# Optimization experiments

Measured on AMD Instinct MI355X. Metric: run time of the kernel, lower is better.

Reference implementation:

```python
import jax, jax.numpy as jnp
import numpy as np

NUM_HEADS = 16
HEAD_DIM = 128
POLY_ORDER = 4
LRPE_BASE = 10000.0
EPS = 1e-6


def _rope(x, offset=0):
    # x: [b, n, h, d] -- Lrpe type-1 rotary position embedding per head dim
    d = x.shape[-1]
    half = d // 2
    theta = LRPE_BASE ** (-jnp.arange(half, dtype=jnp.float32) * 2.0 / d)  # [half]
    pos = jnp.arange(x.shape[1], dtype=jnp.float32) + offset               # [n]
    ang = pos[:, None] * theta[None, :]                                    # [n, half]
    cos = jnp.cos(ang)[None, :, None, :]
    sin = jnp.sin(ang)[None, :, None, :]
    x1, x2 = x[..., :half], x[..., half:]
    return jnp.concatenate([x1 * cos - x2 * sin, x1 * sin + x2 * cos], axis=-1)


def setup_inputs() -> dict:
    key = jax.random.key(0)
    ks = jax.random.split(key, 5)
    b, n, d = 2, 2048, 2048
    std = 0.02  # init_std from module
    x = jax.random.normal(ks[0], (b, n, d), dtype=jnp.float32)
    Wq = jax.random.normal(ks[1], (d, d), dtype=jnp.float32) * std
    Wk = jax.random.normal(ks[2], (d, d), dtype=jnp.float32) * std
    Wv = jax.random.normal(ks[3], (d, d), dtype=jnp.float32) * std
    Wo = jax.random.normal(ks[4], (d, d), dtype=jnp.float32) * std
    return {"x": x, "Wq": Wq, "Wk": Wk, "Wv": Wv, "Wo": Wo}


def reference(x, Wq, Wk, Wv, Wo):
    b, n, d = x.shape
    h, hd = NUM_HEADS, HEAD_DIM
    # projections (nn.Linear: x @ W.T)
    q = (x @ Wq.T).reshape(b, n, h, hd)
    k = (x @ Wk.T).reshape(b, n, h, hd)
    v = (x @ Wv.T).reshape(b, n, h, hd)
    # LRPE (rotary, type 1), offset = 0 (no cache)
    q = _rope(q)
    k = _rope(k)
    # polynomial (non-softmax) attention: scores = (q.k)^p, causal mask,
    # row-normalized (linear-attention-style denominator)
    scores = jnp.einsum("bnhd,bmhd->bhnm", q, k) ** POLY_ORDER  # p=4 even -> >=0
    causal = jnp.tril(jnp.ones((n, n), dtype=scores.dtype))
    scores = scores * causal
    denom = jnp.maximum(scores.sum(-1, keepdims=True), EPS)      # [b,h,n,1]
    out = jnp.einsum("bhnm,bmhd->bhnd", scores, v) / denom        # [b,h,n,hd]
    out = out.transpose(0, 2, 1, 3).reshape(b, n, d)              # b n (h d)
    return out @ Wo.T
```

## Files before the change

kernel.cpp:

```cpp
#include <hip/hip_runtime.h>


typedef __bf16 bf16;
typedef __bf16 bf16x8 __attribute__((ext_vector_type(8)));
typedef __bf16 bf16x4 __attribute__((ext_vector_type(4)));
typedef float f32x4 __attribute__((ext_vector_type(4)));

#define GLD(g, l)                                                   \
  __builtin_amdgcn_global_load_lds(                                 \
      (const __attribute__((address_space(1))) void*)(g),           \
      (__attribute__((address_space(3))) void*)(l), 16, 0, 0)

#define MFMA(a, b, c) __builtin_amdgcn_mfma_f32_16x16x32_bf16(a, b, c, 0, 0, 0)

__global__ __launch_bounds__(256) void k_prep(
    const float* __restrict__ x, const float* __restrict__ Wq,
    const float* __restrict__ Wk, const float* __restrict__ Wv,
    const float* __restrict__ Wo, bf16* __restrict__ xb,
    bf16* __restrict__ wqkv, bf16* __restrict__ wob,
    float* __restrict__ ct, float* __restrict__ st) {
  const int b = blockIdx.x, tid = threadIdx.x;
  if (b < 8192) {
    int i = b * 256 + tid;
    float4 v = reinterpret_cast<const float4*>(x)[i];
    bf16x4 o = {(bf16)v.x, (bf16)v.y, (bf16)v.z, (bf16)v.w};
    reinterpret_cast<bf16x4*>(xb)[i] = o;
  } else if (b < 20480) {
    int i = (b - 8192) * 256 + tid;
    const float* src = (i < 1048576) ? Wq : ((i < 2097152) ? Wk : Wv);
    float4 v = reinterpret_cast<const float4*>(src)[i & 1048575];
    bf16x4 o = {(bf16)v.x, (bf16)v.y, (bf16)v.z, (bf16)v.w};
    reinterpret_cast<bf16x4*>(wqkv)[i] = o;
  } else if (b < 24576) {
    int i = (b - 20480) * 256 + tid;
    float4 v = reinterpret_cast<const float4*>(Wo)[i];
    bf16x4 o = {(bf16)v.x, (bf16)v.y, (bf16)v.z, (bf16)v.w};
    reinterpret_cast<bf16x4*>(wob)[i] = o;
  } else {
    int i = (b - 24576) * 256 + tid;
    int pos = i >> 6, f = i & 63;
    float theta = exp2f(-(float)f * 0.20762050593046014f);
    float ang = (float)pos * theta;
    ct[i] = cosf(ang);
    st[i] = sinf(ang);
  }
}

__global__ __launch_bounds__(256, 2) void k_gemm_qkv(
    const bf16* __restrict__ Am, const bf16* __restrict__ Bm,
    bf16* __restrict__ Qp, bf16* __restrict__ Kp, bf16* __restrict__ Vt,
    const float* __restrict__ ct, const float* __restrict__ st) {
  __shared__ __align__(16) char LDS[73728];
  const int tid = threadIdx.x, w = tid >> 6, l = tid & 63;
  const int lr = l & 15, g = l >> 4;
  const int wr = w >> 1, wc = w & 1;
  const int tm = blockIdx.y * 256, tn = blockIdx.x * 128;

  const int rl = tid >> 2;
  const int scol = (((tid & 3) ^ (rl & 3) ^ ((rl >> 2) & 3)) << 3);
  const int xo = ((g ^ (lr & 3) ^ ((lr >> 2) & 3)) << 4);

#define STAGEQ(buf, kt)                                                      \
  {                                                                          \
    _Pragma("unroll") for (int i = 0; i < 4; ++i)                            \
        GLD(Am + (size_t)(tm + i * 64 + rl) * 2048 + (kt) + scol,            \
            LDS + (buf) * 24576 + i * 4096 + tid * 16);                      \
    _Pragma("unroll") for (int i = 0; i < 2; ++i)                            \
        GLD(Bm + (size_t)(tn + i * 64 + rl) * 2048 + (kt) + scol,            \
            LDS + (buf) * 24576 + 16384 + i * 4096 + tid * 16);              \
  }

  f32x4 acc[8][4] = {};

  STAGEQ(0, 0);
  STAGEQ(1, 32);
  int cur = 0, st3 = 2;
  for (int t = 0; t < 63; ++t) {
    asm volatile("s_waitcnt vmcnt(6)" ::: "memory");
    __builtin_amdgcn_s_barrier();
    asm volatile("" ::: "memory");
    if (t < 62) STAGEQ(st3, (t + 2) * 32);
    const char* pa = LDS + cur * 24576;
    const char* pb = pa + 16384;
    bf16x8 a[8], b[4];
#pragma unroll
    for (int fm = 0; fm < 8; ++fm)
      a[fm] = *reinterpret_cast<const bf16x8*>(pa + (wr * 128 + fm * 16 + lr) * 64 + xo);
#pragma unroll
    for (int nf = 0; nf < 4; ++nf)
      b[nf] = *reinterpret_cast<const bf16x8*>(pb + (wc * 64 + nf * 16 + lr) * 64 + xo);
    __builtin_amdgcn_s_setprio(1);
#pragma unroll
    for (int fm = 0; fm < 8; ++fm)
#pragma unroll
      for (int nf = 0; nf < 4; ++nf)
        acc[fm][nf] = MFMA(a[fm], b[nf], acc[fm][nf]);
    __builtin_amdgcn_s_setprio(0);
    cur = (cur == 2) ? 0 : cur + 1;
    st3 = (st3 == 2) ? 0 : st3 + 1;
  }
  {
    asm volatile("s_waitcnt vmcnt(0)" ::: "memory");
    __builtin_amdgcn_s_barrier();
    asm volatile("" ::: "memory");
    const char* pa = LDS + cur * 24576;
    const char* pb = pa + 16384;
    bf16x8 a[8], b[4];
#pragma unroll
    for (int fm = 0; fm < 8; ++fm)
      a[fm] = *reinterpret_cast<const bf16x8*>(pa + (wr * 128 + fm * 16 + lr) * 64 + xo);
#pragma unroll
    for (int nf = 0; nf < 4; ++nf)
      b[nf] = *reinterpret_cast<const bf16x8*>(pb + (wc * 64 + nf * 16 + lr) * 64 + xo);
#pragma unroll
    for (int fm = 0; fm < 8; ++fm)
#pragma unroll
      for (int nf = 0; nf < 4; ++nf)
        acc[fm][nf] = MFMA(a[fm], b[nf], acc[fm][nf]);
  }

  if (tn < 4096) {
    __syncthreads();
    bf16* E = (bf16*)LDS;
#pragma unroll
    for (int fm = 0; fm < 8; ++fm)
#pragma unroll
      for (int nf = 0; nf < 4; ++nf)
#pragma unroll
        for (int rr = 0; rr < 4; ++rr)
          E[(wr * 128 + fm * 16 + g * 4 + rr) * 136 + wc * 64 + nf * 16 + lr] =
              (bf16)acc[fm][nf][rr];
    __syncthreads();
    const int hh = (tn & 2047) >> 7;
    bf16* dst = (tn < 2048) ? Qp : Kp;
#pragma unroll
    for (int i = 0; i < 16; ++i) {
      int task = i * 256 + tid;
      int row = task >> 4, dg = (task & 15) << 2;
      int token = tm + row, nn = token & 2047, bb = token >> 11;
      f32x4 c4 = *reinterpret_cast<const f32x4*>(ct + nn * 64 + dg);
      f32x4 s4 = *reinterpret_cast<const f32x4*>(st + nn * 64 + dg);
      bf16x4 x1 = *reinterpret_cast<const bf16x4*>(E + row * 136 + dg);
      bf16x4 x2 = *reinterpret_cast<const bf16x4*>(E + row * 136 + 64 + dg);
      bf16x4 o1, o2;
#pragma unroll
      for (int j = 0; j < 4; ++j) {
        float a1 = (float)x1[j], a2 = (float)x2[j];
        o1[j] = (bf16)(a1 * c4[j] - a2 * s4[j]);
        o2[j] = (bf16)(a1 * s4[j] + a2 * c4[j]);
      }
      size_t rb = (((size_t)bb * 16 + hh) * 2048 + nn) * 128;
      *reinterpret_cast<bf16x4*>(dst + rb + dg) = o1;
      *reinterpret_cast<bf16x4*>(dst + rb + 64 + dg) = o2;
    }
  } else {
#pragma unroll
    for (int fm = 0; fm < 8; ++fm)
#pragma unroll
      for (int nf = 0; nf < 4; ++nf) {
        int row0 = tm + wr * 128 + fm * 16 + g * 4;
        int col = (tn - 4096) + wc * 64 + nf * 16 + lr;
        int bb = row0 >> 11, nn = row0 & 2047;
        int hh = col >> 7, dd = col & 127;
        bf16x4 o = {(bf16)acc[fm][nf][0], (bf16)acc[fm][nf][1],
                    (bf16)acc[fm][nf][2], (bf16)acc[fm][nf][3]};
        *reinterpret_cast<bf16x4*>(
            Vt + (((size_t)bb * 16 + hh) * 128 + dd) * 2048 + nn) = o;
      }
  }
}

__global__ __launch_bounds__(256, 3) void k_gemm_out(const bf16* __restrict__ Am,
                                                     const bf16* __restrict__ Bm,
                                                     float* __restrict__ C) {
  __shared__ __align__(16) char LDS[49152];
  const int tid = threadIdx.x, w = tid >> 6, l = tid & 63;
  const int lr = l & 15, g = l >> 4;
  const int wr = w >> 1, wc = w & 1;
  const int tm = blockIdx.y * 128, tn = blockIdx.x * 128;

  const int rl = tid >> 2;
  const int scol = (((tid & 3) ^ (rl & 3) ^ ((rl >> 2) & 3)) << 3);
  const int xo = ((g ^ (lr & 3) ^ ((lr >> 2) & 3)) << 4);

#define STAGEO(buf, kt)                                                      \
  {                                                                          \
    _Pragma("unroll") for (int i = 0; i < 2; ++i)                            \
        GLD(Am + (size_t)(tm + i * 64 + rl) * 2048 + (kt) + scol,            \
            LDS + (buf) * 16384 + i * 4096 + tid * 16);                      \
    _Pragma("unroll") for (int i = 0; i < 2; ++i)                            \
        GLD(Bm + (size_t)(tn + i * 64 + rl) * 2048 + (kt) + scol,            \
            LDS + (buf) * 16384 + 8192 + i * 4096 + tid * 16);               \
  }

  f32x4 acc[4][4] = {};

  STAGEO(0, 0);
  STAGEO(1, 32);
  int cur = 0, st3 = 2;
  for (int t = 0; t < 63; ++t) {
    asm volatile("s_waitcnt vmcnt(4)" ::: "memory");
    __builtin_amdgcn_s_barrier();
    asm volatile("" ::: "memory");
    if (t < 62) STAGEO(st3, (t + 2) * 32);
    const char* pa = LDS + cur * 16384;
    const char* pb = pa + 8192;
    bf16x8 a[4], b[4];
#pragma unroll
    for (int fm = 0; fm < 4; ++fm)
      a[fm] = *reinterpret_cast<const bf16x8*>(pa + (wr * 64 + fm * 16 + lr) * 64 + xo);
#pragma unroll
    for (int nf = 0; nf < 4; ++nf)
      b[nf] = *reinterpret_cast<const bf16x8*>(pb + (wc * 64 + nf * 16 + lr) * 64 + xo);
    __builtin_amdgcn_s_setprio(1);
#pragma unroll
    for (int fm = 0; fm < 4; ++fm)
#pragma unroll
      for (int nf = 0; nf < 4; ++nf)
        acc[fm][nf] = MFMA(a[fm], b[nf], acc[fm][nf]);
    __builtin_amdgcn_s_setprio(0);
    cur = (cur == 2) ? 0 : cur + 1;
    st3 = (st3 == 2) ? 0 : st3 + 1;
  }
  {
    asm volatile("s_waitcnt vmcnt(0)" ::: "memory");
    __builtin_amdgcn_s_barrier();
    asm volatile("" ::: "memory");
    const char* pa = LDS + cur * 16384;
    const char* pb = pa + 8192;
    bf16x8 a[4], b[4];
#pragma unroll
    for (int fm = 0; fm < 4; ++fm)
      a[fm] = *reinterpret_cast<const bf16x8*>(pa + (wr * 64 + fm * 16 + lr) * 64 + xo);
#pragma unroll
    for (int nf = 0; nf < 4; ++nf)
      b[nf] = *reinterpret_cast<const bf16x8*>(pb + (wc * 64 + nf * 16 + lr) * 64 + xo);
#pragma unroll
    for (int fm = 0; fm < 4; ++fm)
#pragma unroll
      for (int nf = 0; nf < 4; ++nf)
        acc[fm][nf] = MFMA(a[fm], b[nf], acc[fm][nf]);
  }

#pragma unroll
  for (int fm = 0; fm < 4; ++fm)
#pragma unroll
    for (int nf = 0; nf < 4; ++nf)
#pragma unroll
      for (int rr = 0; rr < 4; ++rr) {
        int row = tm + wr * 64 + fm * 16 + g * 4 + rr;
        int col = tn + wc * 64 + nf * 16 + lr;
        C[(size_t)row * 2048 + col] = acc[fm][nf][rr];
      }
}

__global__ __launch_bounds__(256) void k_attn(const bf16* __restrict__ Q,
                                              const bf16* __restrict__ K,
                                              const bf16* __restrict__ Vt,
                                              bf16* __restrict__ O) {
  __shared__ __align__(16) bf16 Ks[2][64 * 128];
  __shared__ __align__(16) bf16 Vs[2][128 * 64];
  __shared__ __align__(16) bf16 Ps[128 * 64];
  const int tid = threadIdx.x, w = tid >> 6, l = tid & 63;
  const int lr = l & 15, g = l >> 4;
  const int pair = blockIdx.x >> 5;
  const int bh = blockIdx.x & 31;
  const size_t base = (size_t)bh * 2048 * 128;
  const int b_ = bh >> 4, h_ = bh & 15;

  bf16x8 vones = {};
  if (lr == 0) {
#pragma unroll
    for (int j = 0; j < 8; ++j) vones[j] = (bf16)1.0f;
  }

#define STAGEKV(tt, buf)                                                 \
  {                                                                      \
    const bf16* kg = K + base + (size_t)(tt) * 64 * 128;                 \
    _Pragma("unroll") for (int r = 0; r < 4; ++r) {                      \
      int row = r * 16 + w * 4 + (l >> 4);                               \
      int cc = l & 15;                                                   \
      GLD(kg + (row << 7) + ((cc ^ (row & 7)) << 3),                     \
          Ks[buf] + r * 2048 + w * 512);                                 \
    }                                                                    \
    const bf16* vg = Vt + base + (tt) * 64;                              \
    _Pragma("unroll") for (int r = 0; r < 4; ++r) {                      \
      int row = r * 32 + w * 8 + (l >> 3);                               \
      int cc = l & 7;                                                    \
      GLD(vg + (size_t)row * 2048 + ((cc ^ (row & 7)) << 3),             \
          Vs[buf] + r * 2048 + w * 512);                                 \
    }                                                                    \
  }

  for (int seg = 0; seg < 2; ++seg) {
    const int qb = seg ? (15 - pair) : pair;
    const int qbase = qb * 128;
    const int nt = 2 * qb + 2;

    bf16x8 qf[2][4];
#pragma unroll
    for (int mi = 0; mi < 2; ++mi)
#pragma unroll
      for (int kc = 0; kc < 4; ++kc)
        qf[mi][kc] = *reinterpret_cast<const bf16x8*>(
            Q + base + (size_t)(qbase + w * 32 + mi * 16 + lr) * 128 + kc * 32 + g * 8);

    f32x4 on[2][8] = {};
    f32x4 dn4[2] = {};

    __builtin_amdgcn_s_barrier();
    STAGEKV(0, 0);

    for (int t = 0; t < nt; ++t) {
      int tn1 = (t + 1 < nt) ? t + 1 : nt - 1;
      STAGEKV(tn1, (t + 1) & 1);
      asm volatile("s_waitcnt vmcnt(8)" ::: "memory");
      __builtin_amdgcn_s_barrier();

      const bf16* kcur = Ks[t & 1];
      const bf16* vcur = Vs[t & 1];

      f32x4 s[2][4] = {};
      __builtin_amdgcn_s_setprio(1);
#pragma unroll
      for (int kc = 0; kc < 4; ++kc) {
        bf16x8 kb[4];
#pragma unroll
        for (int ni = 0; ni < 4; ++ni)
          kb[ni] = *reinterpret_cast<const bf16x8*>(
              kcur + ((ni * 16 + lr) << 7) + (((kc * 4 + g) ^ (lr & 7)) << 3));
#pragma unroll
        for (int mi = 0; mi < 2; ++mi)
#pragma unroll
          for (int ni = 0; ni < 4; ++ni)
            s[mi][ni] = MFMA(qf[mi][kc], kb[ni], s[mi][ni]);
      }
      __builtin_amdgcn_s_setprio(0);

#pragma unroll
      for (int mi = 0; mi < 2; ++mi) {
        const bool msk = (t * 64 + 63 > qbase + w * 32 + mi * 16);
#pragma unroll
        for (int ni = 0; ni < 4; ++ni)
#pragma unroll
          for (int r = 0; r < 4; ++r) {
            int lrow = mi * 16 + g * 4 + r;
            float v = s[mi][ni][r];
            if (msk) {
              int qrow = qbase + w * 32 + lrow;
              int col = t * 64 + ni * 16 + lr;
              v = (col <= qrow) ? v : 0.f;
            }
            float v2 = v * v, v4 = v2 * v2;
            Ps[((w * 32 + lrow) << 6) +
               (((ni * 2 + (lr >> 3)) ^ (lrow & 7)) << 3) + (lr & 7)] = (bf16)v4;
          }
      }

      __builtin_amdgcn_s_setprio(1);
#pragma unroll
      for (int k2 = 0; k2 < 2; ++k2) {
        bf16x8 pa[2];
#pragma unroll
        for (int mi = 0; mi < 2; ++mi)
          pa[mi] = *reinterpret_cast<const bf16x8*>(
              Ps + ((w * 32 + mi * 16 + lr) << 6) + (((k2 * 4 + g) ^ (lr & 7)) << 3));
        dn4[0] = MFMA(pa[0], vones, dn4[0]);
        dn4[1] = MFMA(pa[1], vones, dn4[1]);
#pragma unroll
        for (int ni = 0; ni < 8; ++ni) {
          bf16x8 vbf = *reinterpret_cast<const bf16x8*>(
              vcur + ((ni * 16 + lr) << 6) + (((k2 * 4 + g) ^ (lr & 7)) << 3));
          on[0][ni] = MFMA(pa[0], vbf, on[0][ni]);
          on[1][ni] = MFMA(pa[1], vbf, on[1][ni]);
        }
      }
      __builtin_amdgcn_s_setprio(0);
      __builtin_amdgcn_s_barrier();
    }

    asm volatile("s_waitcnt vmcnt(0)" ::: "memory");

#pragma unroll
    for (int mi = 0; mi < 2; ++mi)
#pragma unroll
      for (int r = 0; r < 4; ++r) {
        float d = __shfl(dn4[mi][r], l & 48);
        float inv = 1.0f / fmaxf(d, 1e-6f);
        int row = qbase + w * 32 + mi * 16 + g * 4 + r;
#pragma unroll
        for (int ni = 0; ni < 8; ++ni)
          O[((size_t)b_ * 2048 + row) * 2048 + h_ * 128 + ni * 16 + lr] =
              (bf16)(on[mi][ni][r] * inv);
      }
  }
#undef STAGEKV
}

extern "C" void kernel_launch(void* const* d_in, const int* in_sizes, int n_in,
                              void* d_out, int out_size, void* d_ws, size_t ws_size,
                              hipStream_t stream) {
  const float* x  = (const float*)d_in[0];
  const float* Wq = (const float*)d_in[1];
  const float* Wk = (const float*)d_in[2];
  const float* Wv = (const float*)d_in[3];
  const float* Wo = (const float*)d_in[4];
  float* out = (float*)d_out;

  char* p = (char*)d_ws;
  bf16* xb   = (bf16*)p; p += (size_t)8388608 * 2;
  bf16* wqkv = (bf16*)p; p += (size_t)12582912 * 2;
  bf16* wob  = (bf16*)p; p += (size_t)4194304 * 2;
  bf16* Qp   = (bf16*)p; p += (size_t)8388608 * 2;
  bf16* Kp   = (bf16*)p; p += (size_t)8388608 * 2;
  bf16* Vt   = (bf16*)p; p += (size_t)8388608 * 2;
  bf16* Ob   = (bf16*)p; p += (size_t)8388608 * 2;
  float* ct  = (float*)p; p += (size_t)131072 * 4;
  float* st  = (float*)p; p += (size_t)131072 * 4;

  k_prep<<<25088, 256, 0, stream>>>(x, Wq, Wk, Wv, Wo, xb, wqkv, wob, ct, st);

  k_gemm_qkv<<<dim3(48, 16), 256, 0, stream>>>(xb, wqkv, Qp, Kp, Vt, ct, st);

  k_attn<<<256, 256, 0, stream>>>(Qp, Kp, Vt, Ob);

  k_gemm_out<<<dim3(16, 32), 256, 0, stream>>>(Ob, wob, out);
}
```

Baseline: 243.6 us.

## Split attention KV tiles across two wave groups with LDS reduction

The attention kernel now runs 512 threads per block: two groups of four waves each process alternating 64-key tiles for the same 128 query rows, each group with its own LDS region for K, V and P. V is staged into a single buffer with an extra wait and barrier before the PV MFMAs, while K stays double-buffered. At the end, group 1 writes its partial outputs and denominators to LDS and group 0 sums them, normalizes and writes the result. This doubles the waves per block to hide latency on a 256-block grid, at the cost of 128KB of LDS per block, extra barriers and a reduction epilogue.

```diff
diff --git a/kernel.cpp b/kernel.cpp
--- a/kernel.cpp
+++ b/kernel.cpp
@@ -254,19 +254,19 @@
       }
 }
 
-__global__ __launch_bounds__(256) void k_attn(const bf16* __restrict__ Q,
+__global__ __launch_bounds__(512) void k_attn(const bf16* __restrict__ Q,
                                               const bf16* __restrict__ K,
                                               const bf16* __restrict__ Vt,
                                               bf16* __restrict__ O) {
-  __shared__ __align__(16) bf16 Ks[2][64 * 128];
-  __shared__ __align__(16) bf16 Vs[2][128 * 64];
-  __shared__ __align__(16) bf16 Ps[128 * 64];
+  __shared__ __align__(16) char LDSC[131072];
   const int tid = threadIdx.x, w = tid >> 6, l = tid & 63;
+  const int wg = w & 3, gp = w >> 2;
   const int lr = l & 15, g = l >> 4;
   const int pair = blockIdx.x >> 5;
   const int bh = blockIdx.x & 31;
   const size_t base = (size_t)bh * 2048 * 128;
   const int b_ = bh >> 4, h_ = bh & 15;
+  const int GB = gp * 65536;
 
   bf16x8 vones = {};
   if (lr == 0) {
@@ -274,28 +274,31 @@
     for (int j = 0; j < 8; ++j) vones[j] = (bf16)1.0f;
   }
 
-#define STAGEKV(tt, buf)                                                 \
-  {                                                                      \
-    const bf16* kg = K + base + (size_t)(tt) * 64 * 128;                 \
-    _Pragma("unroll") for (int r = 0; r < 4; ++r) {                      \
-      int row = r * 16 + w * 4 + (l >> 4);                               \
-      int cc = l & 15;                                                   \
-      GLD(kg + (row << 7) + ((cc ^ (row & 7)) << 3),                     \
-          Ks[buf] + r * 2048 + w * 512);                                 \
-    }                                                                    \
-    const bf16* vg = Vt + base + (tt) * 64;                              \
-    _Pragma("unroll") for (int r = 0; r < 4; ++r) {                      \
-      int row = r * 32 + w * 8 + (l >> 3);                               \
-      int cc = l & 7;                                                    \
-      GLD(vg + (size_t)row * 2048 + ((cc ^ (row & 7)) << 3),             \
-          Vs[buf] + r * 2048 + w * 512);                                 \
-    }                                                                    \
+#define STAGE_K(tt, buf)                                                  \
+  {                                                                       \
+    const bf16* kg = K + base + (size_t)(tt) * 64 * 128;                  \
+    _Pragma("unroll") for (int r = 0; r < 4; ++r) {                       \
+      int row = r * 16 + wg * 4 + (l >> 4);                               \
+      int cc = l & 15;                                                    \
+      GLD(kg + (row << 7) + ((cc ^ (row & 7)) << 3),                      \
+          LDSC + GB + (buf) * 16384 + r * 4096 + wg * 1024);              \
+    }                                                                     \
+  }
+#define STAGE_V(tt)                                                       \
+  {                                                                       \
+    const bf16* vg = Vt + base + (tt) * 64;                               \
+    _Pragma("unroll") for (int r = 0; r < 4; ++r) {                       \
+      int row = r * 32 + wg * 8 + (l >> 3);                               \
+      int cc = l & 7;                                                     \
+      GLD(vg + (size_t)row * 2048 + ((cc ^ (row & 7)) << 3),              \
+          LDSC + GB + 32768 + r * 4096 + wg * 1024);                      \
+    }                                                                     \
   }
 
   for (int seg = 0; seg < 2; ++seg) {
     const int qb = seg ? (15 - pair) : pair;
     const int qbase = qb * 128;
-    const int nt = 2 * qb + 2;
+    const int nh = qb + 1;
 
     bf16x8 qf[2][4];
 #pragma unroll
@@ -303,22 +306,25 @@
 #pragma unroll
       for (int kc = 0; kc < 4; ++kc)
         qf[mi][kc] = *reinterpret_cast<const bf16x8*>(
-            Q + base + (size_t)(qbase + w * 32 + mi * 16 + lr) * 128 + kc * 32 + g * 8);
+            Q + base + (size_t)(qbase + wg * 32 + mi * 16 + lr) * 128 + kc * 32 + g * 8);
 
     f32x4 on[2][8] = {};
     f32x4 dn4[2] = {};
 
     __builtin_amdgcn_s_barrier();
-    STAGEKV(0, 0);
-
-    for (int t = 0; t < nt; ++t) {
-      int tn1 = (t + 1 < nt) ? t + 1 : nt - 1;
-      STAGEKV(tn1, (t + 1) & 1);
+    STAGE_K(gp, 0);
+
+    for (int j = 0; j < nh; ++j) {
+      const int t = 2 * j + gp;
+      const int tnx = (j + 1 < nh) ? t + 2 : t;
+      STAGE_V(t);
+      STAGE_K(tnx, (j + 1) & 1);
       asm volatile("s_waitcnt vmcnt(8)" ::: "memory");
       __builtin_amdgcn_s_barrier();
 
-      const bf16* kcur = Ks[t & 1];
-      const bf16* vcur = Vs[t & 1];
+      const bf16* kcur = (const bf16*)(LDSC + GB + (j & 1) * 16384);
+      const bf16* vcur = (const bf16*)(LDSC + GB + 32768);
+      bf16* Ps = (bf16*)(LDSC + GB + 49152);
 
       f32x4 s[2][4] = {};
       __builtin_amdgcn_s_setprio(1);
@@ -339,7 +345,7 @@
 
 #pragma unroll
       for (int mi = 0; mi < 2; ++mi) {
-        const bool msk = (t * 64 + 63 > qbase + w * 32 + mi * 16);
+        const bool msk = (t * 64 + 63 > qbase + wg * 32 + mi * 16);
 #pragma unroll
         for (int ni = 0; ni < 4; ++ni)
 #pragma unroll
@@ -347,16 +353,19 @@
             int lrow = mi * 16 + g * 4 + r;
             float v = s[mi][ni][r];
             if (msk) {
-              int qrow = qbase + w * 32 + lrow;
+              int qrow = qbase + wg * 32 + lrow;
               int col = t * 64 + ni * 16 + lr;
               v = (col <= qrow) ? v : 0.f;
             }
             float v2 = v * v, v4 = v2 * v2;
-            Ps[((w * 32 + lrow) << 6) +
+            Ps[((wg * 32 + lrow) << 6) +
                (((ni * 2 + (lr >> 3)) ^ (lrow & 7)) << 3) + (lr & 7)] = (bf16)v4;
           }
       }
 
+      asm volatile("s_waitcnt vmcnt(4)" ::: "memory");
+      __builtin_amdgcn_s_barrier();
+
       __builtin_amdgcn_s_setprio(1);
 #pragma unroll
       for (int k2 = 0; k2 < 2; ++k2) {
@@ -364,7 +373,7 @@
 #pragma unroll
         for (int mi = 0; mi < 2; ++mi)
           pa[mi] = *reinterpret_cast<const bf16x8*>(
-              Ps + ((w * 32 + mi * 16 + lr) << 6) + (((k2 * 4 + g) ^ (lr & 7)) << 3));
+              Ps + ((wg * 32 + mi * 16 + lr) << 6) + (((k2 * 4 + g) ^ (lr & 7)) << 3));
         dn4[0] = MFMA(pa[0], vones, dn4[0]);
         dn4[1] = MFMA(pa[1], vones, dn4[1]);
 #pragma unroll
@@ -380,21 +389,42 @@
     }
 
     asm volatile("s_waitcnt vmcnt(0)" ::: "memory");
-
-#pragma unroll
-    for (int mi = 0; mi < 2; ++mi)
-#pragma unroll
-      for (int r = 0; r < 4; ++r) {
-        float d = __shfl(dn4[mi][r], l & 48);
-        float inv = 1.0f / fmaxf(d, 1e-6f);
-        int row = qbase + w * 32 + mi * 16 + g * 4 + r;
-#pragma unroll
-        for (int ni = 0; ni < 8; ++ni)
-          O[((size_t)b_ * 2048 + row) * 2048 + h_ * 128 + ni * 16 + lr] =
-              (bf16)(on[mi][ni][r] * inv);
-      }
-  }
-#undef STAGEKV
+    __builtin_amdgcn_s_barrier();
+
+    if (gp == 1) {
+      f32x4* dst = (f32x4*)(LDSC + (size_t)(tid & 255) * 288);
+#pragma unroll
+      for (int mi = 0; mi < 2; ++mi)
+#pragma unroll
+        for (int ni = 0; ni < 8; ++ni) dst[mi * 8 + ni] = on[mi][ni];
+      dst[16] = dn4[0];
+      dst[17] = dn4[1];
+    }
+    __builtin_amdgcn_s_barrier();
+    if (gp == 0) {
+      const f32x4* src = (const f32x4*)(LDSC + (size_t)tid * 288);
+#pragma unroll
+      for (int mi = 0; mi < 2; ++mi)
+#pragma unroll
+        for (int ni = 0; ni < 8; ++ni) on[mi][ni] += src[mi * 8 + ni];
+      dn4[0] += src[16];
+      dn4[1] += src[17];
+#pragma unroll
+      for (int mi = 0; mi < 2; ++mi)
+#pragma unroll
+        for (int r = 0; r < 4; ++r) {
+          float d = __shfl(dn4[mi][r], l & 48);
+          float inv = 1.0f / fmaxf(d, 1e-6f);
+          int row = qbase + wg * 32 + mi * 16 + g * 4 + r;
+#pragma unroll
+          for (int ni = 0; ni < 8; ++ni)
+            O[((size_t)b_ * 2048 + row) * 2048 + h_ * 128 + ni * 16 + lr] =
+                (bf16)(on[mi][ni][r] * inv);
+        }
+    }
+  }
+#undef STAGE_K
+#undef STAGE_V
 }
 
 extern "C" void kernel_launch(void* const* d_in, const int* in_sizes, int n_in,
@@ -422,7 +452,7 @@
 
   k_gemm_qkv<<<dim3(48, 16), 256, 0, stream>>>(xb, wqkv, Qp, Kp, Vt, ct, st);
 
-  k_attn<<<256, 256, 0, stream>>>(Qp, Kp, Vt, Ob);
+  k_attn<<<256, 512, 0, stream>>>(Qp, Kp, Vt, Ob);
 
   k_gemm_out<<<dim3(16, 32), 256, 0, stream>>>(Ob, wob, out);
 }
```

Result: faster. 225.5 us (-7.4%).
